# Optimization experiments

Measured on AMD Instinct MI355X. Metric: run time of the kernel, lower is better.

The kernel has to match this reference:

```python
import jax, jax.numpy as jnp
import numpy as np

TAU = 0.1
MASK_VAL = 1e9


def setup_inputs() -> dict:
    key = jax.random.key(0)
    ka, kb = jax.random.split(key)
    B, D = 4096, 512
    return {
        "view_a": jax.random.normal(ka, (B, D), dtype=jnp.float32),
        "view_b": jax.random.normal(kb, (B, D), dtype=jnp.float32),
    }


def _l2norm(x):
    return x / jnp.maximum(jnp.linalg.norm(x, axis=-1, keepdims=True), 1e-12)


def reference(view_a, view_b):
    a = _l2norm(view_a)
    b = _l2norm(view_b)
    B = a.shape[0]
    labels = jnp.arange(B)  # start_i = 0 (single device)
    mask = jnp.eye(B, dtype=a.dtype) * MASK_VAL

    logits_aa = a @ a.T / TAU - mask
    logits_bb = b @ b.T / TAU - mask
    logits_ab = a @ b.T / TAU
    logits_ba = b @ a.T / TAU

    full_a = jnp.concatenate([logits_ab, logits_aa], axis=1)  # [B, 2B]
    full_b = jnp.concatenate([logits_ba, logits_bb], axis=1)

    def ce(logits):
        logp = jax.nn.log_softmax(logits, axis=-1)
        return -jnp.mean(jnp.take_along_axis(logp, labels[:, None], axis=-1))

    loss = (ce(full_a) + ce(full_b)) / 2

    pred = jnp.argmax(full_a, axis=-1)
    acc = 100.0 * jnp.sum(pred == labels) / B
    return loss, acc
```

## Files before the change

### kernel.cpp

```cpp
#include <hip/hip_runtime.h>
#include <stdint.h>


#define BN 4096
#define DK 512
#define NEG_BIG -1e30f

typedef __attribute__((ext_vector_type(8))) __bf16 bf16x8;
typedef __attribute__((ext_vector_type(4))) float floatx4;

__device__ __forceinline__ unsigned short f2bf(float f) {
  unsigned int u = __float_as_uint(f);
  u += 0x7fffu + ((u >> 16) & 1u);
  return (unsigned short)(u >> 16);
}

__global__ void zero_kernel(float* out) {
  if (threadIdx.x < 2) out[threadIdx.x] = 0.0f;
}

__global__ void __launch_bounds__(128) prep_kernel(
    const float* __restrict__ A, const float* __restrict__ Bv,
    unsigned short* __restrict__ An, unsigned short* __restrict__ Bn,
    float* __restrict__ diag) {
  const int row = blockIdx.x;
  const int tid = threadIdx.x;
  float4 va = ((const float4*)(A + (size_t)row * DK))[tid];
  float4 vb = ((const float4*)(Bv + (size_t)row * DK))[tid];
  float ssa = va.x * va.x + va.y * va.y + va.z * va.z + va.w * va.w;
  float ssb = vb.x * vb.x + vb.y * vb.y + vb.z * vb.z + vb.w * vb.w;
  float sab = va.x * vb.x + va.y * vb.y + va.z * vb.z + va.w * vb.w;
#pragma unroll
  for (int off = 32; off > 0; off >>= 1) {
    ssa += __shfl_xor(ssa, off);
    ssb += __shfl_xor(ssb, off);
    sab += __shfl_xor(sab, off);
  }
  __shared__ float red[3][2];
  if ((tid & 63) == 0) {
    int w = tid >> 6;
    red[0][w] = ssa; red[1][w] = ssb; red[2][w] = sab;
  }
  __syncthreads();
  ssa = red[0][0] + red[0][1];
  ssb = red[1][0] + red[1][1];
  sab = red[2][0] + red[2][1];
  float na = fmaxf(sqrtf(ssa), 1e-12f);
  float nb = fmaxf(sqrtf(ssb), 1e-12f);
  const float S = 3.16227766016838f;
  float sa = S / na, sb = S / nb;
  ushort4 pa, pb;
  pa.x = f2bf(va.x * sa); pa.y = f2bf(va.y * sa);
  pa.z = f2bf(va.z * sa); pa.w = f2bf(va.w * sa);
  pb.x = f2bf(vb.x * sb); pb.y = f2bf(vb.y * sb);
  pb.z = f2bf(vb.z * sb); pb.w = f2bf(vb.w * sb);
  ((ushort4*)(An + (size_t)row * DK))[tid] = pa;
  ((ushort4*)(Bn + (size_t)row * DK))[tid] = pb;
  if (tid == 0) diag[row] = (sab / (na * nb)) * 10.0f;
}

__global__ void __launch_bounds__(256, 2) tiles_kernel(
    const unsigned short* __restrict__ An, const unsigned short* __restrict__ Bn,
    float* __restrict__ pmA, float* __restrict__ plA,
    float* __restrict__ pmB, float* __restrict__ plB) {
  __shared__ __align__(16) unsigned short tile[64 * DK];

  const int rb = blockIdx.x;
  const int split = blockIdx.y;
  const int tid = threadIdx.x;
  const int lane = tid & 63, w = tid >> 6;
  const int n = lane & 15, q = lane >> 4;
  const int r0 = rb * 64;

  bf16x8 afA[16], afB[16];
  {
    const int row = r0 + w * 16 + n;
    const unsigned short* pa = An + (size_t)row * DK + q * 8;
    const unsigned short* pb = Bn + (size_t)row * DK + q * 8;
#pragma unroll
    for (int kc = 0; kc < 16; ++kc) {
      afA[kc] = *(const bf16x8*)(pa + kc * 32);
      afB[kc] = *(const bf16x8*)(pb + kc * 32);
    }
  }

  float mA[4], lA[4], mB[4], lB[4];
#pragma unroll
  for (int r = 0; r < 4; ++r) { mA[r] = NEG_BIG; lA[r] = 0.f; mB[r] = NEG_BIG; lB[r] = 0.f; }

  for (int t = 0; t < 16; ++t) {
    const int jt = split * 16 + t;
    __syncthreads();
    {
      const int cbase = jt * 64;
#pragma unroll
      for (int i = 0; i < 16; ++i) {
        const int cl = w * 16 + i;
        const int c = cbase + cl;
        const unsigned short* src =
            (c < BN) ? (An + (size_t)c * DK) : (Bn + (size_t)(c - BN) * DK);
        const int sw = (lane ^ (cl & 7)) * 8;
        __builtin_amdgcn_global_load_lds(
            (const __attribute__((address_space(1))) void*)(src + sw),
            (__attribute__((address_space(3))) void*)(&tile[cl * DK]),
            16, 0, 0);
      }
    }
    __syncthreads();

    floatx4 accA[4], accB[4];
#pragma unroll
    for (int cs = 0; cs < 4; ++cs) {
      floatx4 z = {0.f, 0.f, 0.f, 0.f};
      accA[cs] = z; accB[cs] = z;
    }
    const int nx = n & 7;
#pragma unroll
    for (int kc = 0; kc < 16; ++kc) {
#pragma unroll
      for (int cs = 0; cs < 4; ++cs) {
        const int col = cs * 16 + n;
        const int phys = ((kc * 4 + q) ^ nx) * 8;
        bf16x8 bfr = *(const bf16x8*)(tile + col * DK + phys);
        accA[cs] = __builtin_amdgcn_mfma_f32_16x16x32_bf16(afA[kc], bfr, accA[cs], 0, 0, 0);
        accB[cs] = __builtin_amdgcn_mfma_f32_16x16x32_bf16(afB[kc], bfr, accB[cs], 0, 0, 0);
      }
    }

    if (jt == rb || jt == rb + 64) {
#pragma unroll
      for (int cs = 0; cs < 4; ++cs)
#pragma unroll
        for (int r = 0; r < 4; ++r) {
          bool kill = (cs == w) && (n == q * 4 + r);
          if (kill) { accA[cs][r] = NEG_BIG; accB[cs][r] = NEG_BIG; }
        }
    }

#pragma unroll
    for (int r = 0; r < 4; ++r) {
      {
        float a0 = accA[0][r], a1 = accA[1][r], a2 = accA[2][r], a3 = accA[3][r];
        float vmax = fmaxf(fmaxf(a0, a1), fmaxf(a2, a3));
        float mn = fmaxf(mA[r], vmax);
        float s = __expf(a0 - mn) + __expf(a1 - mn) + __expf(a2 - mn) + __expf(a3 - mn);
        lA[r] = lA[r] * __expf(mA[r] - mn) + s;
        mA[r] = mn;
      }
      {
        float b0 = accB[0][r], b1 = accB[1][r], b2 = accB[2][r], b3 = accB[3][r];
        float vmax = fmaxf(fmaxf(b0, b1), fmaxf(b2, b3));
        float mn = fmaxf(mB[r], vmax);
        float s = __expf(b0 - mn) + __expf(b1 - mn) + __expf(b2 - mn) + __expf(b3 - mn);
        lB[r] = lB[r] * __expf(mB[r] - mn) + s;
        mB[r] = mn;
      }
    }
  }

#pragma unroll
  for (int off = 1; off < 16; off <<= 1) {
#pragma unroll
    for (int r = 0; r < 4; ++r) {
      float mo = __shfl_xor(mA[r], off), lo = __shfl_xor(lA[r], off);
      float mn = fmaxf(mA[r], mo);
      lA[r] = lA[r] * __expf(mA[r] - mn) + lo * __expf(mo - mn);
      mA[r] = mn;
      mo = __shfl_xor(mB[r], off); lo = __shfl_xor(lB[r], off);
      mn = fmaxf(mB[r], mo);
      lB[r] = lB[r] * __expf(mB[r] - mn) + lo * __expf(mo - mn);
      mB[r] = mn;
    }
  }
  if (n == 0) {
    const int base = split * BN + r0 + w * 16 + q * 4;
#pragma unroll
    for (int r = 0; r < 4; ++r) {
      pmA[base + r] = mA[r];
      plA[base + r] = lA[r];
      pmB[base + r] = mB[r];
      plB[base + r] = lB[r];
    }
  }
}

__global__ void __launch_bounds__(256) finalize_kernel(
    const float* __restrict__ pmA, const float* __restrict__ plA,
    const float* __restrict__ pmB, const float* __restrict__ plB,
    const float* __restrict__ diag, float* __restrict__ out) {
  const int row = blockIdx.x * 256 + threadIdx.x;
  float Ma = NEG_BIG, La = 0.f, Mb = NEG_BIG, Lb = 0.f;
#pragma unroll
  for (int s = 0; s < 8; ++s) {
    float m = pmA[s * BN + row], l = plA[s * BN + row];
    float mn = fmaxf(Ma, m);
    La = La * __expf(Ma - mn) + l * __expf(m - mn);
    Ma = mn;
    m = pmB[s * BN + row]; l = plB[s * BN + row];
    mn = fmaxf(Mb, m);
    Lb = Lb * __expf(Mb - mn) + l * __expf(m - mn);
    Mb = mn;
  }
  const float d = diag[row];
  float corr = (d >= Ma) ? 1.f : 0.f;
  float mna = fmaxf(Ma, d);
  float lseA = mna + logf(La * __expf(Ma - mna) + __expf(d - mna));
  float mnb = fmaxf(Mb, d);
  float lseB = mnb + logf(Lb * __expf(Mb - mnb) + __expf(d - mnb));
  float lossi = (lseA - d) + (lseB - d);
#pragma unroll
  for (int off = 32; off > 0; off >>= 1) {
    lossi += __shfl_xor(lossi, off);
    corr += __shfl_xor(corr, off);
  }
  __shared__ float sred[2][4];
  if ((threadIdx.x & 63) == 0) {
    int w = threadIdx.x >> 6;
    sred[0][w] = lossi; sred[1][w] = corr;
  }
  __syncthreads();
  if (threadIdx.x == 0) {
    float ls = sred[0][0] + sred[0][1] + sred[0][2] + sred[0][3];
    float cs = sred[1][0] + sred[1][1] + sred[1][2] + sred[1][3];
    atomicAdd(&out[0], ls * (1.0f / 8192.0f));
    atomicAdd(&out[1], cs * (100.0f / 4096.0f));
  }
}

extern "C" void kernel_launch(void* const* d_in, const int* in_sizes, int n_in,
                              void* d_out, int out_size, void* d_ws, size_t ws_size,
                              hipStream_t stream) {
  const float* A = (const float*)d_in[0];
  const float* Bv = (const float*)d_in[1];
  unsigned short* An = (unsigned short*)d_ws;
  unsigned short* Bn = An + (size_t)BN * DK;
  float* diag = (float*)(Bn + (size_t)BN * DK);
  float* pmA = diag + BN;
  float* plA = pmA + 8 * BN;
  float* pmB = plA + 8 * BN;
  float* plB = pmB + 8 * BN;
  float* out = (float*)d_out;

  zero_kernel<<<1, 64, 0, stream>>>(out);
  prep_kernel<<<BN, 128, 0, stream>>>(A, Bv, An, Bn, diag);
  tiles_kernel<<<dim3(64, 8), 256, 0, stream>>>(An, Bn, pmA, plA, pmB, plB);
  finalize_kernel<<<16, 256, 0, stream>>>(pmA, plA, pmB, plB, diag, out);
}
```

Before: 139.3 us.

## Exploit Gram-matrix symmetry with triangular tile grid and column-wise softmax partials

Exploits the symmetry of a·aᵀ, b·bᵀ and a·bᵀ/b·aᵀ by launching only upper-triangular 64x64 block pairs. Each tile computes both row-wise and column-wise online max/sum partials, so the mirrored tile never has to be computed. This roughly halves the MFMA work. In exchange it adds column reductions through shuffles and shared memory, and grows the partial buffers to 64 splits, which the finalize kernel must merge. The zero kernel is also folded into the prep kernel to save a launch.

```diff
diff --git a/kernel.cpp b/kernel.cpp
--- a/kernel.cpp
+++ b/kernel.cpp
@@ -4,6 +4,7 @@
 
 #define BN 4096
 #define DK 512
+#define NB 64
 #define NEG_BIG -1e30f
 
 typedef __attribute__((ext_vector_type(8))) __bf16 bf16x8;
@@ -15,14 +16,17 @@
   return (unsigned short)(u >> 16);
 }
 
-__global__ void zero_kernel(float* out) {
-  if (threadIdx.x < 2) out[threadIdx.x] = 0.0f;
+__device__ __forceinline__ void mlmerge(float& m, float& l, float m2, float l2) {
+  float mn = fmaxf(m, m2);
+  l = l * __expf(m - mn) + l2 * __expf(m2 - mn);
+  m = mn;
 }
 
 __global__ void __launch_bounds__(128) prep_kernel(
     const float* __restrict__ A, const float* __restrict__ Bv,
     unsigned short* __restrict__ An, unsigned short* __restrict__ Bn,
-    float* __restrict__ diag) {
+    float* __restrict__ diag, float* __restrict__ out) {
+  if (blockIdx.x == 0 && threadIdx.x < 2) out[threadIdx.x] = 0.0f;
   const int row = blockIdx.x;
   const int tid = threadIdx.x;
   float4 va = ((const float4*)(A + (size_t)row * DK))[tid];
@@ -65,16 +69,20 @@
     float* __restrict__ pmB, float* __restrict__ plB) {
   __shared__ __align__(16) unsigned short tile[64 * DK];
 
-  const int rb = blockIdx.x;
-  const int split = blockIdx.y;
+  int idx = blockIdx.x;
+  int bi = 0;
+  while (idx >= NB - bi) { idx -= NB - bi; ++bi; }
+  const int bj = bi + idx;
+  const bool diag = (bi == bj);
+
   const int tid = threadIdx.x;
   const int lane = tid & 63, w = tid >> 6;
   const int n = lane & 15, q = lane >> 4;
-  const int r0 = rb * 64;
+  const int r0i = bi * 64, r0j = bj * 64;
 
   bf16x8 afA[16], afB[16];
   {
-    const int row = r0 + w * 16 + n;
+    const int row = r0i + w * 16 + n;
     const unsigned short* pa = An + (size_t)row * DK + q * 8;
     const unsigned short* pb = Bn + (size_t)row * DK + q * 8;
 #pragma unroll
@@ -84,27 +92,26 @@
     }
   }
 
-  float mA[4], lA[4], mB[4], lB[4];
-#pragma unroll
-  for (int r = 0; r < 4; ++r) { mA[r] = NEG_BIG; lA[r] = 0.f; mB[r] = NEG_BIG; lB[r] = 0.f; }
-
-  for (int t = 0; t < 16; ++t) {
-    const int jt = split * 16 + t;
+  float mRa[4], lRa[4], mRb[4], lRb[4];
+#pragma unroll
+  for (int r = 0; r < 4; ++r) { mRa[r] = NEG_BIG; lRa[r] = 0.f; mRb[r] = NEG_BIG; lRb[r] = 0.f; }
+
+  float mC0[4], lC0[4], mC1[4], lC1[4];
+
+  const int nx = n & 7;
+
+  for (int t = 0; t < 2; ++t) {
+    const unsigned short* colsrc = (t == 0) ? An : Bn;
     __syncthreads();
-    {
-      const int cbase = jt * 64;
-#pragma unroll
-      for (int i = 0; i < 16; ++i) {
-        const int cl = w * 16 + i;
-        const int c = cbase + cl;
-        const unsigned short* src =
-            (c < BN) ? (An + (size_t)c * DK) : (Bn + (size_t)(c - BN) * DK);
-        const int sw = (lane ^ (cl & 7)) * 8;
-        __builtin_amdgcn_global_load_lds(
-            (const __attribute__((address_space(1))) void*)(src + sw),
-            (__attribute__((address_space(3))) void*)(&tile[cl * DK]),
-            16, 0, 0);
-      }
+#pragma unroll
+    for (int ii = 0; ii < 16; ++ii) {
+      const int cl = w * 16 + ii;
+      const unsigned short* src = colsrc + (size_t)(r0j + cl) * DK;
+      const int sw = (lane ^ (cl & 7)) * 8;
+      __builtin_amdgcn_global_load_lds(
+          (const __attribute__((address_space(1))) void*)(src + sw),
+          (__attribute__((address_space(3))) void*)(&tile[cl * DK]),
+          16, 0, 0);
     }
     __syncthreads();
 
@@ -114,7 +121,6 @@
       floatx4 z = {0.f, 0.f, 0.f, 0.f};
       accA[cs] = z; accB[cs] = z;
     }
-    const int nx = n & 7;
 #pragma unroll
     for (int kc = 0; kc < 16; ++kc) {
 #pragma unroll
@@ -127,33 +133,78 @@
       }
     }
 
-    if (jt == rb || jt == rb + 64) {
+    if (diag) {
 #pragma unroll
       for (int cs = 0; cs < 4; ++cs)
 #pragma unroll
-        for (int r = 0; r < 4; ++r) {
-          bool kill = (cs == w) && (n == q * 4 + r);
-          if (kill) { accA[cs][r] = NEG_BIG; accB[cs][r] = NEG_BIG; }
-        }
-    }
-
-#pragma unroll
-    for (int r = 0; r < 4; ++r) {
-      {
+        for (int r = 0; r < 4; ++r)
+          if (cs == w && n == q * 4 + r) { accA[cs][r] = NEG_BIG; accB[cs][r] = NEG_BIG; }
+    }
+
+    if (!(diag && t == 1)) {
+#pragma unroll
+      for (int r = 0; r < 4; ++r) {
         float a0 = accA[0][r], a1 = accA[1][r], a2 = accA[2][r], a3 = accA[3][r];
         float vmax = fmaxf(fmaxf(a0, a1), fmaxf(a2, a3));
-        float mn = fmaxf(mA[r], vmax);
+        float mn = fmaxf(mRa[r], vmax);
         float s = __expf(a0 - mn) + __expf(a1 - mn) + __expf(a2 - mn) + __expf(a3 - mn);
-        lA[r] = lA[r] * __expf(mA[r] - mn) + s;
-        mA[r] = mn;
-      }
-      {
-        float b0 = accB[0][r], b1 = accB[1][r], b2 = accB[2][r], b3 = accB[3][r];
-        float vmax = fmaxf(fmaxf(b0, b1), fmaxf(b2, b3));
-        float mn = fmaxf(mB[r], vmax);
-        float s = __expf(b0 - mn) + __expf(b1 - mn) + __expf(b2 - mn) + __expf(b3 - mn);
-        lB[r] = lB[r] * __expf(mB[r] - mn) + s;
-        mB[r] = mn;
+        lRa[r] = lRa[r] * __expf(mRa[r] - mn) + s;
+        mRa[r] = mn;
+      }
+    }
+#pragma unroll
+    for (int r = 0; r < 4; ++r) {
+      float b0 = accB[0][r], b1 = accB[1][r], b2 = accB[2][r], b3 = accB[3][r];
+      float vmax = fmaxf(fmaxf(b0, b1), fmaxf(b2, b3));
+      float mn = fmaxf(mRb[r], vmax);
+      float s = __expf(b0 - mn) + __expf(b1 - mn) + __expf(b2 - mn) + __expf(b3 - mn);
+      lRb[r] = lRb[r] * __expf(mRb[r] - mn) + s;
+      mRb[r] = mn;
+    }
+
+    if (t == 0) {
+#pragma unroll
+      for (int cs = 0; cs < 4; ++cs) {
+        float m = NEG_BIG;
+        if (!diag) {
+#pragma unroll
+          for (int r = 0; r < 4; ++r) m = fmaxf(m, accA[cs][r]);
+        }
+#pragma unroll
+        for (int r = 0; r < 4; ++r) m = fmaxf(m, accB[cs][r]);
+        float l = 0.f;
+        if (!diag) {
+#pragma unroll
+          for (int r = 0; r < 4; ++r) l += __expf(accA[cs][r] - m);
+        }
+#pragma unroll
+        for (int r = 0; r < 4; ++r) l += __expf(accB[cs][r] - m);
+#pragma unroll
+        for (int off = 16; off < 64; off <<= 1) {
+          float mo = __shfl_xor(m, off), lo = __shfl_xor(l, off);
+          float mn = fmaxf(m, mo);
+          l = l * __expf(m - mn) + lo * __expf(mo - mn);
+          m = mn;
+        }
+        mC0[cs] = m; lC0[cs] = l;
+      }
+    } else if (!diag) {
+#pragma unroll
+      for (int cs = 0; cs < 4; ++cs) {
+        float m = NEG_BIG;
+#pragma unroll
+        for (int r = 0; r < 4; ++r) m = fmaxf(fmaxf(m, accA[cs][r]), accB[cs][r]);
+        float l = 0.f;
+#pragma unroll
+        for (int r = 0; r < 4; ++r) l += __expf(accA[cs][r] - m) + __expf(accB[cs][r] - m);
+#pragma unroll
+        for (int off = 16; off < 64; off <<= 1) {
+          float mo = __shfl_xor(m, off), lo = __shfl_xor(l, off);
+          float mn = fmaxf(m, mo);
+          l = l * __expf(m - mn) + lo * __expf(mo - mn);
+          m = mn;
+        }
+        mC1[cs] = m; lC1[cs] = l;
       }
     }
   }
@@ -162,24 +213,72 @@
   for (int off = 1; off < 16; off <<= 1) {
 #pragma unroll
     for (int r = 0; r < 4; ++r) {
-      float mo = __shfl_xor(mA[r], off), lo = __shfl_xor(lA[r], off);
-      float mn = fmaxf(mA[r], mo);
-      lA[r] = lA[r] * __expf(mA[r] - mn) + lo * __expf(mo - mn);
-      mA[r] = mn;
-      mo = __shfl_xor(mB[r], off); lo = __shfl_xor(lB[r], off);
-      mn = fmaxf(mB[r], mo);
-      lB[r] = lB[r] * __expf(mB[r] - mn) + lo * __expf(mo - mn);
-      mB[r] = mn;
+      float mo = __shfl_xor(mRa[r], off), lo = __shfl_xor(lRa[r], off);
+      float mn = fmaxf(mRa[r], mo);
+      lRa[r] = lRa[r] * __expf(mRa[r] - mn) + lo * __expf(mo - mn);
+      mRa[r] = mn;
+      mo = __shfl_xor(mRb[r], off); lo = __shfl_xor(lRb[r], off);
+      mn = fmaxf(mRb[r], mo);
+      lRb[r] = lRb[r] * __expf(mRb[r] - mn) + lo * __expf(mo - mn);
+      mRb[r] = mn;
+    }
+  }
+
+  __syncthreads();
+  float* colbuf = (float*)tile;
+  float* rowbuf = colbuf + 2 * 4 * 64 * 2;
+
+  if (q == 0) {
+#pragma unroll
+    for (int cs = 0; cs < 4; ++cs) {
+      const int c = cs * 16 + n;
+      colbuf[((0 * 4 + w) * 64 + c) * 2 + 0] = mC0[cs];
+      colbuf[((0 * 4 + w) * 64 + c) * 2 + 1] = lC0[cs];
+      if (!diag) {
+        colbuf[((1 * 4 + w) * 64 + c) * 2 + 0] = mC1[cs];
+        colbuf[((1 * 4 + w) * 64 + c) * 2 + 1] = lC1[cs];
+      }
     }
   }
   if (n == 0) {
-    const int base = split * BN + r0 + w * 16 + q * 4;
 #pragma unroll
     for (int r = 0; r < 4; ++r) {
-      pmA[base + r] = mA[r];
-      plA[base + r] = lA[r];
-      pmB[base + r] = mB[r];
-      plB[base + r] = lB[r];
+      const int rr = w * 16 + q * 4 + r;
+      rowbuf[(0 * 64 + rr) * 2 + 0] = mRa[r];
+      rowbuf[(0 * 64 + rr) * 2 + 1] = lRa[r];
+      rowbuf[(1 * 64 + rr) * 2 + 0] = mRb[r];
+      rowbuf[(1 * 64 + rr) * 2 + 1] = lRb[r];
+    }
+  }
+  __syncthreads();
+
+  if (tid < 128) {
+    const int prob = tid >> 6, tt = tid & 63;
+    float* pm = prob ? pmB : pmA;
+    float* pl = prob ? plB : plA;
+    float rm = rowbuf[(prob * 64 + tt) * 2 + 0];
+    float rl = rowbuf[(prob * 64 + tt) * 2 + 1];
+    if (diag) {
+      if (prob == 0) {
+        float cm = NEG_BIG, cl2 = 0.f;
+#pragma unroll
+        for (int wv = 0; wv < 4; ++wv)
+          mlmerge(cm, cl2, colbuf[((0 * 4 + wv) * 64 + tt) * 2 + 0],
+                           colbuf[((0 * 4 + wv) * 64 + tt) * 2 + 1]);
+        mlmerge(rm, rl, cm, cl2);
+      }
+      pm[(size_t)bi * BN + r0i + tt] = rm;
+      pl[(size_t)bi * BN + r0i + tt] = rl;
+    } else {
+      float cm = NEG_BIG, cl2 = 0.f;
+#pragma unroll
+      for (int wv = 0; wv < 4; ++wv)
+        mlmerge(cm, cl2, colbuf[((prob * 4 + wv) * 64 + tt) * 2 + 0],
+                         colbuf[((prob * 4 + wv) * 64 + tt) * 2 + 1]);
+      pm[(size_t)bj * BN + r0i + tt] = rm;
+      pl[(size_t)bj * BN + r0i + tt] = rl;
+      pm[(size_t)bi * BN + r0j + tt] = cm;
+      pl[(size_t)bi * BN + r0j + tt] = cl2;
     }
   }
 }
@@ -190,16 +289,10 @@
     const float* __restrict__ diag, float* __restrict__ out) {
   const int row = blockIdx.x * 256 + threadIdx.x;
   float Ma = NEG_BIG, La = 0.f, Mb = NEG_BIG, Lb = 0.f;
-#pragma unroll
-  for (int s = 0; s < 8; ++s) {
-    float m = pmA[s * BN + row], l = plA[s * BN + row];
-    float mn = fmaxf(Ma, m);
-    La = La * __expf(Ma - mn) + l * __expf(m - mn);
-    Ma = mn;
-    m = pmB[s * BN + row]; l = plB[s * BN + row];
-    mn = fmaxf(Mb, m);
-    Lb = Lb * __expf(Mb - mn) + l * __expf(m - mn);
-    Mb = mn;
+#pragma unroll 4
+  for (int s = 0; s < NB; ++s) {
+    mlmerge(Ma, La, pmA[(size_t)s * BN + row], plA[(size_t)s * BN + row]);
+    mlmerge(Mb, Lb, pmB[(size_t)s * BN + row], plB[(size_t)s * BN + row]);
   }
   const float d = diag[row];
   float corr = (d >= Ma) ? 1.f : 0.f;
@@ -236,13 +329,12 @@
   unsigned short* Bn = An + (size_t)BN * DK;
   float* diag = (float*)(Bn + (size_t)BN * DK);
   float* pmA = diag + BN;
-  float* plA = pmA + 8 * BN;
-  float* pmB = plA + 8 * BN;
-  float* plB = pmB + 8 * BN;
+  float* plA = pmA + (size_t)NB * BN;
+  float* pmB = plA + (size_t)NB * BN;
+  float* plB = pmB + (size_t)NB * BN;
   float* out = (float*)d_out;
 
-  zero_kernel<<<1, 64, 0, stream>>>(out);
-  prep_kernel<<<BN, 128, 0, stream>>>(A, Bv, An, Bn, diag);
-  tiles_kernel<<<dim3(64, 8), 256, 0, stream>>>(An, Bn, pmA, plA, pmB, plB);
-  finalize_kernel<<<16, 256, 0, stream>>>(pmA, plA, pmB, plB, diag, out);
-}
+  prep_kernel<<<BN, 128, 0, stream>>>(A, Bv, An, Bn, diag, out);
+  tiles_kernel<<<NB * (NB + 1) / 2, 256, 0, stream>>>(An, Bn, pmA, plA, pmB, plB);
+  finalize_kernel<<<BN / 256, 256, 0, stream>>>(pmA, plA, pmB, plB, diag, out);
+}
```

New measurement: 239.3 us. 1.72x slower.

## Use 32x32 MFMA with 128-row blocks and double-buffered LDS column tiles

Applied to the files above, without the earlier changes.

The tiles kernel now handles 128 rows per block with 32x32x16 bf16 MFMAs instead of 16x16x32. Each B fragment read from LDS is reused across more output rows, which cuts LDS traffic per MFMA. The next column tile is prefetched into a second LDS buffer while the current one is computed, removing one barrier per iteration and overlapping loads with compute. The prep kernel now uses one wave per row and also zeroes the output, so the separate zero kernel launch is gone. In exchange, register pressure and LDS use rise sharply (128 KB dynamic LDS, one block per CU), and the grid is halved to 256 blocks, which lowers occupancy and latency hiding.

```diff
diff --git a/kernel.cpp b/kernel.cpp
--- a/kernel.cpp
+++ b/kernel.cpp
@@ -4,10 +4,12 @@
 
 #define BN 4096
 #define DK 512
+#define NSPLIT 8
 #define NEG_BIG -1e30f
+#define TILE_ELEMS (64 * DK)
 
 typedef __attribute__((ext_vector_type(8))) __bf16 bf16x8;
-typedef __attribute__((ext_vector_type(4))) float floatx4;
+typedef __attribute__((ext_vector_type(16))) float floatx16;
 
 __device__ __forceinline__ unsigned short f2bf(float f) {
   unsigned int u = __float_as_uint(f);
@@ -15,171 +17,172 @@
   return (unsigned short)(u >> 16);
 }
 
-__global__ void zero_kernel(float* out) {
-  if (threadIdx.x < 2) out[threadIdx.x] = 0.0f;
-}
-
-__global__ void __launch_bounds__(128) prep_kernel(
+__device__ __forceinline__ void mlmerge(float& m, float& l, float m2, float l2) {
+  float mn = fmaxf(m, m2);
+  l = l * __expf(m - mn) + l2 * __expf(m2 - mn);
+  m = mn;
+}
+
+__global__ void __launch_bounds__(256) prep_kernel(
     const float* __restrict__ A, const float* __restrict__ Bv,
     unsigned short* __restrict__ An, unsigned short* __restrict__ Bn,
-    float* __restrict__ diag) {
-  const int row = blockIdx.x;
-  const int tid = threadIdx.x;
-  float4 va = ((const float4*)(A + (size_t)row * DK))[tid];
-  float4 vb = ((const float4*)(Bv + (size_t)row * DK))[tid];
-  float ssa = va.x * va.x + va.y * va.y + va.z * va.z + va.w * va.w;
-  float ssb = vb.x * vb.x + vb.y * vb.y + vb.z * vb.z + vb.w * vb.w;
-  float sab = va.x * vb.x + va.y * vb.y + va.z * vb.z + va.w * vb.w;
+    float* __restrict__ diag, float* __restrict__ out) {
+  if (blockIdx.x == 0 && threadIdx.x < 2) out[threadIdx.x] = 0.0f;
+  const int w = threadIdx.x >> 6, lane = threadIdx.x & 63;
+  const int row = blockIdx.x * 4 + w;
+  const float4* pa4 = (const float4*)(A + (size_t)row * DK);
+  const float4* pb4 = (const float4*)(Bv + (size_t)row * DK);
+  float4 a0 = pa4[lane], a1 = pa4[lane + 64];
+  float4 b0 = pb4[lane], b1 = pb4[lane + 64];
+  float ssa = a0.x * a0.x + a0.y * a0.y + a0.z * a0.z + a0.w * a0.w +
+              a1.x * a1.x + a1.y * a1.y + a1.z * a1.z + a1.w * a1.w;
+  float ssb = b0.x * b0.x + b0.y * b0.y + b0.z * b0.z + b0.w * b0.w +
+              b1.x * b1.x + b1.y * b1.y + b1.z * b1.z + b1.w * b1.w;
+  float sab = a0.x * b0.x + a0.y * b0.y + a0.z * b0.z + a0.w * b0.w +
+              a1.x * b1.x + a1.y * b1.y + a1.z * b1.z + a1.w * b1.w;
 #pragma unroll
   for (int off = 32; off > 0; off >>= 1) {
     ssa += __shfl_xor(ssa, off);
     ssb += __shfl_xor(ssb, off);
     sab += __shfl_xor(sab, off);
   }
-  __shared__ float red[3][2];
-  if ((tid & 63) == 0) {
-    int w = tid >> 6;
-    red[0][w] = ssa; red[1][w] = ssb; red[2][w] = sab;
-  }
-  __syncthreads();
-  ssa = red[0][0] + red[0][1];
-  ssb = red[1][0] + red[1][1];
-  sab = red[2][0] + red[2][1];
   float na = fmaxf(sqrtf(ssa), 1e-12f);
   float nb = fmaxf(sqrtf(ssb), 1e-12f);
   const float S = 3.16227766016838f;
   float sa = S / na, sb = S / nb;
-  ushort4 pa, pb;
-  pa.x = f2bf(va.x * sa); pa.y = f2bf(va.y * sa);
-  pa.z = f2bf(va.z * sa); pa.w = f2bf(va.w * sa);
-  pb.x = f2bf(vb.x * sb); pb.y = f2bf(vb.y * sb);
-  pb.z = f2bf(vb.z * sb); pb.w = f2bf(vb.w * sb);
-  ((ushort4*)(An + (size_t)row * DK))[tid] = pa;
-  ((ushort4*)(Bn + (size_t)row * DK))[tid] = pb;
-  if (tid == 0) diag[row] = (sab / (na * nb)) * 10.0f;
-}
-
-__global__ void __launch_bounds__(256, 2) tiles_kernel(
+  ushort4 p;
+  p.x = f2bf(a0.x * sa); p.y = f2bf(a0.y * sa); p.z = f2bf(a0.z * sa); p.w = f2bf(a0.w * sa);
+  ((ushort4*)(An + (size_t)row * DK))[lane] = p;
+  p.x = f2bf(a1.x * sa); p.y = f2bf(a1.y * sa); p.z = f2bf(a1.z * sa); p.w = f2bf(a1.w * sa);
+  ((ushort4*)(An + (size_t)row * DK))[lane + 64] = p;
+  p.x = f2bf(b0.x * sb); p.y = f2bf(b0.y * sb); p.z = f2bf(b0.z * sb); p.w = f2bf(b0.w * sb);
+  ((ushort4*)(Bn + (size_t)row * DK))[lane] = p;
+  p.x = f2bf(b1.x * sb); p.y = f2bf(b1.y * sb); p.z = f2bf(b1.z * sb); p.w = f2bf(b1.w * sb);
+  ((ushort4*)(Bn + (size_t)row * DK))[lane + 64] = p;
+  if (lane == 0) diag[row] = (sab / (na * nb)) * 10.0f;
+}
+
+__global__ void __launch_bounds__(256, 1) tiles_kernel(
     const unsigned short* __restrict__ An, const unsigned short* __restrict__ Bn,
     float* __restrict__ pmA, float* __restrict__ plA,
     float* __restrict__ pmB, float* __restrict__ plB) {
-  __shared__ __align__(16) unsigned short tile[64 * DK];
+  extern __shared__ __align__(16) unsigned short smem[];
 
   const int rb = blockIdx.x;
   const int split = blockIdx.y;
   const int tid = threadIdx.x;
   const int lane = tid & 63, w = tid >> 6;
-  const int n = lane & 15, q = lane >> 4;
-  const int r0 = rb * 64;
-
-  bf16x8 afA[16], afB[16];
+  const int n5 = lane & 31, h = lane >> 5, nx = n5 & 7;
+  const int r0 = rb * 128;
+
+  bf16x8 afA[32], afB[32];
   {
-    const int row = r0 + w * 16 + n;
-    const unsigned short* pa = An + (size_t)row * DK + q * 8;
-    const unsigned short* pb = Bn + (size_t)row * DK + q * 8;
-#pragma unroll
-    for (int kc = 0; kc < 16; ++kc) {
-      afA[kc] = *(const bf16x8*)(pa + kc * 32);
-      afB[kc] = *(const bf16x8*)(pb + kc * 32);
-    }
-  }
-
-  float mA[4], lA[4], mB[4], lB[4];
-#pragma unroll
-  for (int r = 0; r < 4; ++r) { mA[r] = NEG_BIG; lA[r] = 0.f; mB[r] = NEG_BIG; lB[r] = 0.f; }
+    const int myrow = r0 + w * 32 + n5;
+    const unsigned short* pa = An + (size_t)myrow * DK + h * 8;
+    const unsigned short* pb = Bn + (size_t)myrow * DK + h * 8;
+#pragma unroll
+    for (int kc = 0; kc < 32; ++kc) {
+      afA[kc] = *(const bf16x8*)(pa + kc * 16);
+      afB[kc] = *(const bf16x8*)(pb + kc * 16);
+    }
+  }
+
+  float mA[16], lA[16], mB[16], lB[16];
+#pragma unroll
+  for (int r = 0; r < 16; ++r) { mA[r] = NEG_BIG; lA[r] = 0.f; mB[r] = NEG_BIG; lB[r] = 0.f; }
+
+  auto stage = [&](unsigned short* buf, int jt) {
+    const unsigned short* csrc = (jt < 64) ? An : Bn;
+    const int cb = (jt & 63) * 64;
+#pragma unroll
+    for (int ii = 0; ii < 16; ++ii) {
+      const int cl = w * 16 + ii;
+      const unsigned short* src =
+          csrc + (size_t)(cb + cl) * DK + ((lane ^ (cl & 7)) * 8);
+      __builtin_amdgcn_global_load_lds(
+          (const __attribute__((address_space(1))) void*)src,
+          (__attribute__((address_space(3))) void*)(buf + cl * DK),
+          16, 0, 0);
+    }
+  };
+
+  stage(smem, split * 16);
+  __syncthreads();
 
   for (int t = 0; t < 16; ++t) {
     const int jt = split * 16 + t;
-    __syncthreads();
-    {
-      const int cbase = jt * 64;
-#pragma unroll
-      for (int i = 0; i < 16; ++i) {
-        const int cl = w * 16 + i;
-        const int c = cbase + cl;
-        const unsigned short* src =
-            (c < BN) ? (An + (size_t)c * DK) : (Bn + (size_t)(c - BN) * DK);
-        const int sw = (lane ^ (cl & 7)) * 8;
-        __builtin_amdgcn_global_load_lds(
-            (const __attribute__((address_space(1))) void*)(src + sw),
-            (__attribute__((address_space(3))) void*)(&tile[cl * DK]),
-            16, 0, 0);
+    unsigned short* cur = smem + (t & 1) * TILE_ELEMS;
+    unsigned short* nxt = smem + ((t + 1) & 1) * TILE_ELEMS;
+    if (t < 15) stage(nxt, jt + 1);
+
+    floatx16 accA[2], accB[2];
+#pragma unroll
+    for (int cs = 0; cs < 2; ++cs)
+#pragma unroll
+      for (int r = 0; r < 16; ++r) { accA[cs][r] = 0.f; accB[cs][r] = 0.f; }
+
+    const unsigned short* b0 = cur + (size_t)n5 * DK;
+#pragma unroll
+    for (int kc = 0; kc < 32; ++kc) {
+      const int chunk = ((kc * 2 + h) ^ nx) * 8;
+      bf16x8 bf0 = *(const bf16x8*)(b0 + chunk);
+      bf16x8 bf1 = *(const bf16x8*)(b0 + 32 * DK + chunk);
+      accA[0] = __builtin_amdgcn_mfma_f32_32x32x16_bf16(afA[kc], bf0, accA[0], 0, 0, 0);
+      accB[0] = __builtin_amdgcn_mfma_f32_32x32x16_bf16(afB[kc], bf0, accB[0], 0, 0, 0);
+      accA[1] = __builtin_amdgcn_mfma_f32_32x32x16_bf16(afA[kc], bf1, accA[1], 0, 0, 0);
+      accB[1] = __builtin_amdgcn_mfma_f32_32x32x16_bf16(afB[kc], bf1, accB[1], 0, 0, 0);
+    }
+
+    if (((jt & 63) >> 1) == rb) {
+      const int colbase = (jt & 63) * 64;
+#pragma unroll
+      for (int cs = 0; cs < 2; ++cs) {
+        const int col = colbase + cs * 32 + n5;
+#pragma unroll
+        for (int r = 0; r < 16; ++r) {
+          const int row = r0 + w * 32 + (r & 3) + 8 * (r >> 2) + 4 * h;
+          if (row == col) { accA[cs][r] = NEG_BIG; accB[cs][r] = NEG_BIG; }
+        }
       }
     }
-    __syncthreads();
-
-    floatx4 accA[4], accB[4];
-#pragma unroll
-    for (int cs = 0; cs < 4; ++cs) {
-      floatx4 z = {0.f, 0.f, 0.f, 0.f};
-      accA[cs] = z; accB[cs] = z;
-    }
-    const int nx = n & 7;
-#pragma unroll
-    for (int kc = 0; kc < 16; ++kc) {
-#pragma unroll
-      for (int cs = 0; cs < 4; ++cs) {
-        const int col = cs * 16 + n;
-        const int phys = ((kc * 4 + q) ^ nx) * 8;
-        bf16x8 bfr = *(const bf16x8*)(tile + col * DK + phys);
-        accA[cs] = __builtin_amdgcn_mfma_f32_16x16x32_bf16(afA[kc], bfr, accA[cs], 0, 0, 0);
-        accB[cs] = __builtin_amdgcn_mfma_f32_16x16x32_bf16(afB[kc], bfr, accB[cs], 0, 0, 0);
-      }
-    }
-
-    if (jt == rb || jt == rb + 64) {
-#pragma unroll
-      for (int cs = 0; cs < 4; ++cs)
-#pragma unroll
-        for (int r = 0; r < 4; ++r) {
-          bool kill = (cs == w) && (n == q * 4 + r);
-          if (kill) { accA[cs][r] = NEG_BIG; accB[cs][r] = NEG_BIG; }
-        }
-    }
-
-#pragma unroll
-    for (int r = 0; r < 4; ++r) {
+
+#pragma unroll
+    for (int r = 0; r < 16; ++r) {
       {
-        float a0 = accA[0][r], a1 = accA[1][r], a2 = accA[2][r], a3 = accA[3][r];
-        float vmax = fmaxf(fmaxf(a0, a1), fmaxf(a2, a3));
-        float mn = fmaxf(mA[r], vmax);
-        float s = __expf(a0 - mn) + __expf(a1 - mn) + __expf(a2 - mn) + __expf(a3 - mn);
-        lA[r] = lA[r] * __expf(mA[r] - mn) + s;
+        float a0 = accA[0][r], a1 = accA[1][r];
+        float mn = fmaxf(mA[r], fmaxf(a0, a1));
+        lA[r] = lA[r] * __expf(mA[r] - mn) + __expf(a0 - mn) + __expf(a1 - mn);
         mA[r] = mn;
       }
       {
-        float b0 = accB[0][r], b1 = accB[1][r], b2 = accB[2][r], b3 = accB[3][r];
-        float vmax = fmaxf(fmaxf(b0, b1), fmaxf(b2, b3));
-        float mn = fmaxf(mB[r], vmax);
-        float s = __expf(b0 - mn) + __expf(b1 - mn) + __expf(b2 - mn) + __expf(b3 - mn);
-        lB[r] = lB[r] * __expf(mB[r] - mn) + s;
+        float v0 = accB[0][r], v1 = accB[1][r];
+        float mn = fmaxf(mB[r], fmaxf(v0, v1));
+        lB[r] = lB[r] * __expf(mB[r] - mn) + __expf(v0 - mn) + __expf(v1 - mn);
         mB[r] = mn;
       }
     }
-  }
-
-#pragma unroll
-  for (int off = 1; off < 16; off <<= 1) {
-#pragma unroll
-    for (int r = 0; r < 4; ++r) {
+    __syncthreads();
+  }
+
+#pragma unroll
+  for (int off = 1; off < 32; off <<= 1) {
+#pragma unroll
+    for (int r = 0; r < 16; ++r) {
       float mo = __shfl_xor(mA[r], off), lo = __shfl_xor(lA[r], off);
-      float mn = fmaxf(mA[r], mo);
-      lA[r] = lA[r] * __expf(mA[r] - mn) + lo * __expf(mo - mn);
-      mA[r] = mn;
+      mlmerge(mA[r], lA[r], mo, lo);
       mo = __shfl_xor(mB[r], off); lo = __shfl_xor(lB[r], off);
-      mn = fmaxf(mB[r], mo);
-      lB[r] = lB[r] * __expf(mB[r] - mn) + lo * __expf(mo - mn);
-      mB[r] = mn;
-    }
-  }
-  if (n == 0) {
-    const int base = split * BN + r0 + w * 16 + q * 4;
-#pragma unroll
-    for (int r = 0; r < 4; ++r) {
-      pmA[base + r] = mA[r];
-      plA[base + r] = lA[r];
-      pmB[base + r] = mB[r];
-      plB[base + r] = lB[r];
+      mlmerge(mB[r], lB[r], mo, lo);
+    }
+  }
+  if (n5 == 0) {
+    const int base = split * BN;
+#pragma unroll
+    for (int r = 0; r < 16; ++r) {
+      const int row = r0 + w * 32 + (r & 3) + 8 * (r >> 2) + 4 * h;
+      pmA[base + row] = mA[r];
+      plA[base + row] = lA[r];
+      pmB[base + row] = mB[r];
+      plB[base + row] = lB[r];
     }
   }
 }
@@ -191,15 +194,9 @@
   const int row = blockIdx.x * 256 + threadIdx.x;
   float Ma = NEG_BIG, La = 0.f, Mb = NEG_BIG, Lb = 0.f;
 #pragma unroll
-  for (int s = 0; s < 8; ++s) {
-    float m = pmA[s * BN + row], l = plA[s * BN + row];
-    float mn = fmaxf(Ma, m);
-    La = La * __expf(Ma - mn) + l * __expf(m - mn);
-    Ma = mn;
-    m = pmB[s * BN + row]; l = plB[s * BN + row];
-    mn = fmaxf(Mb, m);
-    Lb = Lb * __expf(Mb - mn) + l * __expf(m - mn);
-    Mb = mn;
+  for (int s = 0; s < NSPLIT; ++s) {
+    mlmerge(Ma, La, pmA[s * BN + row], plA[s * BN + row]);
+    mlmerge(Mb, Lb, pmB[s * BN + row], plB[s * BN + row]);
   }
   const float d = diag[row];
   float corr = (d >= Ma) ? 1.f : 0.f;
@@ -236,13 +233,13 @@
   unsigned short* Bn = An + (size_t)BN * DK;
   float* diag = (float*)(Bn + (size_t)BN * DK);
   float* pmA = diag + BN;
-  float* plA = pmA + 8 * BN;
-  float* pmB = plA + 8 * BN;
-  float* plB = pmB + 8 * BN;
+  float* plA = pmA + NSPLIT * BN;
+  float* pmB = plA + NSPLIT * BN;
+  float* plB = pmB + NSPLIT * BN;
   float* out = (float*)d_out;
 
-  zero_kernel<<<1, 64, 0, stream>>>(out);
-  prep_kernel<<<BN, 128, 0, stream>>>(A, Bv, An, Bn, diag);
-  tiles_kernel<<<dim3(64, 8), 256, 0, stream>>>(An, Bn, pmA, plA, pmB, plB);
-  finalize_kernel<<<16, 256, 0, stream>>>(pmA, plA, pmB, plB, diag, out);
-}
+  prep_kernel<<<BN / 4, 256, 0, stream>>>(A, Bv, An, Bn, diag, out);
+  tiles_kernel<<<dim3(32, 8), 256, 2 * TILE_ELEMS * sizeof(unsigned short), stream>>>(
+      An, Bn, pmA, plA, pmB, plB);
+  finalize_kernel<<<BN / 256, 256, 0, stream>>>(pmA, plA, pmB, plB, diag, out);
+}
```

New measurement: 159.7 us. 14.7% more time.
